# Optimization experiments

Hardware: AMD Instinct MI355X
Metric: run time of the kernel (lower is better)

Reference implementation:

```python
import jax, jax.numpy as jnp
import numpy as np

B, T, D, H = 2, 2048, 512, 8
HD = D // H
EPS = 1e-5


def setup_inputs() -> dict:
    key = jax.random.key(0)
    ks = jax.random.split(key, 8)
    s = 1.0 / np.sqrt(D)
    return {
        "x": jax.random.normal(ks[0], (B, T, D), dtype=jnp.float32),
        "Wq": jax.random.uniform(ks[1], (D, D), jnp.float32, -s, s),
        "bq": jnp.zeros((D,), jnp.float32),
        "Wk": jax.random.uniform(ks[2], (D, D), jnp.float32, -s, s),
        "bk": jnp.zeros((D,), jnp.float32),
        "Wv": jax.random.uniform(ks[3], (D, D), jnp.float32, -s, s),
        "bv": jnp.zeros((D,), jnp.float32),
        "gn_w": jnp.ones((D,), jnp.float32),
        "gn_b": jnp.zeros((D,), jnp.float32),
        "gamma": jnp.float32(0.9),
    }


def reference(x, Wq, bq, Wk, bk, Wv, bv, gn_w, gn_b, gamma):
    Bx, Tx, Dx = x.shape
    # projections (torch Linear: x @ W.T + b), split heads -> [B,H,T,hd]
    def proj(W, b):
        return (x @ W.T + b).reshape(Bx, Tx, H, HD).transpose(0, 2, 1, 3)
    Q, K, V = proj(Wq, bq), proj(Wk, bk), proj(Wv, bv)
    # retention scores with causal exponential decay mask
    attn = jnp.einsum("bhqd,bhkd->bhqk", Q, K)  # [B,H,T,T]
    idx = jnp.arange(Tx)
    diff = idx[:, None] - idx[None, :]
    # clamp negative exponents before pow to avoid inf (masked out anyway)
    decay = jnp.where(diff >= 0,
                      jnp.power(gamma, jnp.maximum(diff, 0).astype(jnp.float32)),
                      0.0)
    attn = attn * decay[None, None]
    out = jnp.einsum("bhqk,bhkd->bhqd", attn, V)  # [B,H,T,hd]
    out = out.transpose(0, 2, 1, 3)  # [B,T,H,hd]
    # GroupNorm over channels grouped by head; normalized over (T, hd) per (b, h)
    mean = out.mean(axis=(1, 3), keepdims=True)
    var = out.var(axis=(1, 3), keepdims=True)
    out = (out - mean) / jnp.sqrt(var + EPS)
    out = out.reshape(Bx, Tx, Dx) * gn_w + gn_b
    return out
```

## Files before the change

kernel.cpp:

```cpp
#include <hip/hip_runtime.h>
#include <math.h>

#define B_ 2
#define T_ 2048
#define D_ 512
#define H_ 8
#define HD_ 64
#define NG_ (B_*H_)
#define EPS_ 1e-5f

typedef __attribute__((ext_vector_type(8)))  short  short8;
typedef __attribute__((ext_vector_type(16))) float  floatx16;

__device__ inline floatx16 zero16() {
    floatx16 z;
#pragma unroll
    for (int i = 0; i < 16; i++) z[i] = 0.f;
    return z;
}

__device__ inline unsigned pack2bf(float a, float b) {
    unsigned ua = __float_as_uint(a), ub = __float_as_uint(b);
    ua = (ua + 0x7fffu + ((ua >> 16) & 1u)) >> 16;
    ub = (ub + 0x7fffu + ((ub >> 16) & 1u)) >> 16;
    return ua | (ub << 16);
}
__device__ inline short bf1(float a) {
    unsigned ua = __float_as_uint(a);
    return (short)((ua + 0x7fffu + ((ua >> 16) & 1u)) >> 16);
}
__device__ inline uint4 pack8bf(const float4& a, const float4& b) {
    uint4 o;
    o.x = pack2bf(a.x, a.y); o.y = pack2bf(a.z, a.w);
    o.z = pack2bf(b.x, b.y); o.w = pack2bf(b.z, b.w);
    return o;
}

__global__ __launch_bounds__(256, 3) void proj_mfma(
    const float* __restrict__ x,
    const float* __restrict__ Wq, const float* __restrict__ Wk, const float* __restrict__ Wv,
    const float* __restrict__ bq, const float* __restrict__ bk, const float* __restrict__ bv,
    short* __restrict__ Qo, short* __restrict__ Ko, short* __restrict__ Vto,
    float* __restrict__ stats)
{
    __shared__ short Xs[2][64 * 64];
    __shared__ short Ws2[2][128 * 64];

    const int tid = threadIdx.x;
    if (blockIdx.x == 0 && blockIdx.y == 0 && blockIdx.z == 0 && tid < 32)
        stats[tid] = 0.f;

    const int w = tid >> 6, lane = tid & 63;
    const int hi = lane >> 5, ln = lane & 31;
    const int mt0 = blockIdx.x * 64;
    const int nt0 = blockIdx.y * 128;
    const int z = blockIdx.z;
    const bool isV = (z == 2);
    const float* bias = (z == 0) ? bq : (z == 1) ? bk : bv;
    const float* Wz = (z == 0) ? Wq : (z == 1) ? Wk : Wv;

    const int srow = tid >> 3;
    const int scol = (((tid & 7) ^ ((tid >> 3) & 7)) * 8);
    const int mh = w & 1, nh = w >> 1;

    floatx16 acc[2] = {zero16(), zero16()};
    float4 xr[2][2];
    float4 wr[4][2];

    auto gload = [&](int k0) {
#pragma unroll
        for (int i = 0; i < 2; i++) {
            const float* p = x + (size_t)(mt0 + srow + i * 32) * 512 + k0 + scol;
            xr[i][0] = *(const float4*)p;
            xr[i][1] = *(const float4*)(p + 4);
        }
#pragma unroll
        for (int i = 0; i < 4; i++) {
            const float* p = Wz + (size_t)(nt0 + srow + i * 32) * 512 + k0 + scol;
            wr[i][0] = *(const float4*)p;
            wr[i][1] = *(const float4*)(p + 4);
        }
    };
    auto spill = [&](int b) {
        const int slot = (tid & 7) * 8;
#pragma unroll
        for (int i = 0; i < 2; i++)
            *(uint4*)&Xs[b][(srow + i * 32) * 64 + slot] = pack8bf(xr[i][0], xr[i][1]);
#pragma unroll
        for (int i = 0; i < 4; i++)
            *(uint4*)&Ws2[b][(srow + i * 32) * 64 + slot] = pack8bf(wr[i][0], wr[i][1]);
    };

    gload(0);
    int buf = 0;
    for (int k0 = 0; k0 < 512; k0 += 64, buf ^= 1) {
        spill(buf);
        __syncthreads();
        if (k0 + 64 < 512) gload(k0 + 64);
#pragma unroll
        for (int kk = 0; kk < 4; kk++) {
            const int gx = ((2 * kk + hi) ^ (ln & 7)) * 8;
            short8 xf = *(const short8*)(&Xs[buf][(mh * 32 + ln) * 64 + gx]);
            short8 wf[2];
#pragma unroll
            for (int s = 0; s < 2; s++)
                wf[s] = *(const short8*)(&Ws2[buf][(nh * 64 + s * 32 + ln) * 64 + gx]);
#pragma unroll
            for (int b = 0; b < 2; b++)
                acc[b] = isV
                    ? __builtin_amdgcn_mfma_f32_32x32x16_bf16(wf[b], xf, acc[b], 0, 0, 0)
                    : __builtin_amdgcn_mfma_f32_32x32x16_bf16(xf, wf[b], acc[b], 0, 0, 0);
        }
        __syncthreads();
    }

    const int head = blockIdx.y * 2 + nh;

    if (!isV) {
        short* dst = (z == 0) ? Qo : Ko;
        float bias_v[2];
#pragma unroll
        for (int b = 0; b < 2; b++) bias_v[b] = bias[nt0 + nh * 64 + b * 32 + ln];
#pragma unroll
        for (int r = 0; r < 16; r++) {
            int m = mt0 + mh * 32 + (r & 3) + 8 * (r >> 2) + 4 * hi;
            int batch = m >> 11, t = m & (T_ - 1);
            size_t rowb = ((size_t)(batch * H_ + head) * T_ + t) * HD_;
#pragma unroll
            for (int b = 0; b < 2; b++)
                dst[rowb + b * 32 + ln] = bf1(acc[b][r] + bias_v[b]);
        }
    } else {
        const int m = mt0 + mh * 32 + ln;
        const int batch = m >> 11, t = m & (T_ - 1);
#pragma unroll
        for (int b = 0; b < 2; b++) {
#pragma unroll
            for (int r = 0; r < 16; r++) {
                int chan = nt0 + nh * 64 + b * 32 + (r & 3) + 8 * (r >> 2) + 4 * hi;
                int d = chan & (HD_ - 1);
                Vto[((size_t)(batch * H_ + head) * HD_ + d) * T_ + t] = bf1(acc[b][r] + bias[chan]);
            }
        }
    }
}

__global__ __launch_bounds__(256, 2) void retention_kernel(
    const short* __restrict__ Q, const short* __restrict__ K, const short* __restrict__ Vt,
    const float* __restrict__ gamma_p,
    float* __restrict__ out,
    float* __restrict__ stats)
{
    __shared__ float red[3][32 * 64];

    const int tid  = threadIdx.x;
    const int ks   = tid >> 6, lane = tid & 63;
    const int hi   = lane >> 5, ln = lane & 31;
    const int g    = blockIdx.x, qtt = blockIdx.y;
    const int q0   = qtt * 32;
    const int qt   = qtt >> 1;

    const float gamma = gamma_p[0];
    const float lg = logf(gamma);
    int kt0 = 0;
    if (lg < -1e-6f) {
        int maxd = (int)(-13.0f / lg) + 64;
        kt0 = qt - (maxd >> 6);
        if (kt0 < 0) kt0 = 0;
    }

    const short* Qbase = Q + ((size_t)g * T_ + q0 + ln) * HD_;
    short8 qf[4];
#pragma unroll
    for (int c = 0; c < 4; c++) qf[c] = *(const short8*)(Qbase + 16 * c + 8 * hi);

    const float Alane = __expf(lg * (float)(ln - 4 * hi));
    const float G32   = __expf(-lg * 32.0f);
    float Ea[4], Eb[4];
#pragma unroll
    for (int j = 0; j < 4; j++) { Ea[j] = __expf(-lg * (float)j); Eb[j] = __expf(-lg * (float)(8 * j)); }
    const int qrel = (qtt & 1) * 32 + ln;

    floatx16 oacc[2] = {zero16(), zero16()};

    int kt = kt0 + ((ks - kt0) & 3);
    short8 kf[2][4];
    if (kt <= qt) {
        const short* Kbase = K + ((size_t)g * T_ + kt * 64) * HD_;
#pragma unroll
        for (int kh = 0; kh < 2; kh++)
#pragma unroll
            for (int c = 0; c < 4; c++)
                kf[kh][c] = *(const short8*)(Kbase + (size_t)(kh * 32 + ln) * HD_ + 16 * c + 8 * hi);
    }

    for (; kt <= qt; kt += 4) {
        const int k0 = kt * 64;

        floatx16 st[2];
#pragma unroll
        for (int kh = 0; kh < 2; kh++) {
            floatx16 acc = zero16();
#pragma unroll
            for (int c = 0; c < 4; c++)
                acc = __builtin_amdgcn_mfma_f32_32x32x16_bf16(kf[kh][c], qf[c], acc, 0, 0, 0);
            st[kh] = acc;
        }

        short8 vf[4][2];
#pragma unroll
        for (int c = 0; c < 4; c++)
#pragma unroll
            for (int dh = 0; dh < 2; dh++)
                vf[c][dh] = *(const short8*)(Vt + ((size_t)g * HD_ + dh * 32 + ln) * T_ + k0 + 16 * c + 8 * hi);

        const int ktn = kt + 4;
        if (ktn <= qt) {
            const short* Kn = K + ((size_t)g * T_ + ktn * 64) * HD_;
#pragma unroll
            for (int kh = 0; kh < 2; kh++)
#pragma unroll
                for (int c = 0; c < 4; c++)
                    kf[kh][c] = *(const short8*)(Kn + (size_t)(kh * 32 + ln) * HD_ + 16 * c + 8 * hi);
        }

        const float Ckt = __expf(lg * (float)(q0 - k0));
        const float base0 = Alane * Ckt;
        const bool diag = (kt == qt);
#pragma unroll
        for (int kh = 0; kh < 2; kh++) {
            float bb = base0 * (kh ? G32 : 1.0f);
#pragma unroll
            for (int r = 0; r < 16; r++) {
                float v = st[kh][r] * (bb * Ea[r & 3] * Eb[r >> 2]);
                if (diag) {
                    int kloc = kh * 32 + (r & 3) + 8 * (r >> 2) + 4 * hi;
                    if (qrel < kloc) v = 0.f;
                }
                st[kh][r] = v;
            }
        }

#pragma unroll
        for (int c = 0; c < 4; c++) {
            const int kh = c >> 1, rb = 8 * (c & 1);
            unsigned p0 = pack2bf(st[kh][rb+0], st[kh][rb+1]);
            unsigned p1 = pack2bf(st[kh][rb+2], st[kh][rb+3]);
            unsigned p2 = pack2bf(st[kh][rb+4], st[kh][rb+5]);
            unsigned p3 = pack2bf(st[kh][rb+6], st[kh][rb+7]);
            unsigned t0s = (unsigned)__shfl_xor((int)(hi ? p0 : p2), 32, 64);
            unsigned t1s = (unsigned)__shfl_xor((int)(hi ? p1 : p3), 32, 64);
            uint4 aw;
            aw.x = hi ? t0s : p0;  aw.y = hi ? t1s : p1;
            aw.z = hi ? p2  : t0s; aw.w = hi ? p3  : t1s;
            short8 afr = *reinterpret_cast<short8*>(&aw);
#pragma unroll
            for (int dh = 0; dh < 2; dh++)
                oacc[dh] = __builtin_amdgcn_mfma_f32_32x32x16_bf16(afr, vf[c][dh], oacc[dh], 0, 0, 0);
        }
    }

    if (ks) {
        float* rp = &red[ks - 1][0];
#pragma unroll
        for (int dh = 0; dh < 2; dh++)
#pragma unroll
            for (int r = 0; r < 16; r++) {
                int qloc = (r & 3) + 8 * (r >> 2) + 4 * hi;
                rp[qloc * 64 + dh * 32 + ln] = oacc[dh][r];
            }
    }
    __syncthreads();
    if (ks == 0) {
        const int b = g >> 3, h = g & 7;
        float sm = 0.f, sq = 0.f;
#pragma unroll
        for (int dh = 0; dh < 2; dh++)
#pragma unroll
            for (int r = 0; r < 16; r++) {
                int qloc = (r & 3) + 8 * (r >> 2) + 4 * hi;
                int col = qloc * 64 + dh * 32 + ln;
                float v = oacc[dh][r] + red[0][col] + red[1][col] + red[2][col];
                int q = q0 + qloc;
                out[((size_t)(b * T_ + q)) * D_ + h * 64 + dh * 32 + ln] = v;
                sm += v; sq += v * v;
            }
        for (int off = 32; off > 0; off >>= 1) {
            sm += __shfl_down(sm, off);
            sq += __shfl_down(sq, off);
        }
        if (lane == 0) {
            atomicAdd(&stats[g], sm);
            atomicAdd(&stats[NG_ + g], sq);
        }
    }
}

__global__ __launch_bounds__(256) void norm_kernel(
    float* __restrict__ out, const float* __restrict__ stats,
    const float* __restrict__ gn_w, const float* __restrict__ gn_b)
{
    int idx4 = blockIdx.x * 256 + threadIdx.x;
    if (idx4 >= (B_ * T_ * D_) / 4) return;
    int base = idx4 * 4;
    int c0 = base & (D_ - 1);
    int b = base >> 20;
    int g = b * H_ + (c0 >> 6);
    const float invN = 1.f / (float)(T_ * HD_);
    float mean = stats[g] * invN;
    float var  = stats[NG_ + g] * invN - mean * mean;
    float inv  = rsqrtf(var + EPS_);
    float4 v = *(float4*)&out[base];
    float4 wv = *(const float4*)&gn_w[c0];
    float4 bv = *(const float4*)&gn_b[c0];
    v.x = (v.x - mean) * inv * wv.x + bv.x;
    v.y = (v.y - mean) * inv * wv.y + bv.y;
    v.z = (v.z - mean) * inv * wv.z + bv.z;
    v.w = (v.w - mean) * inv * wv.w + bv.w;
    *(float4*)&out[base] = v;
}

extern "C" void kernel_launch(void* const* d_in, const int* in_sizes, int n_in,
                              void* d_out, int out_size, void* d_ws, size_t ws_size,
                              hipStream_t stream)
{
    const float* x    = (const float*)d_in[0];
    const float* Wq   = (const float*)d_in[1];
    const float* bq   = (const float*)d_in[2];
    const float* Wk   = (const float*)d_in[3];
    const float* bk   = (const float*)d_in[4];
    const float* Wv   = (const float*)d_in[5];
    const float* bv   = (const float*)d_in[6];
    const float* gn_w = (const float*)d_in[7];
    const float* gn_b = (const float*)d_in[8];
    const float* gam  = (const float*)d_in[9];
    float* out = (float*)d_out;

    const size_t per = (size_t)B_ * H_ * T_ * HD_;
    float* stats = (float*)d_ws;
    short* Qw  = (short*)((char*)d_ws + 256);
    short* Kw  = Qw + per;
    short* Vtw = Kw + per;

    proj_mfma<<<dim3(64, 4, 3), 256, 0, stream>>>(x, Wq, Wk, Wv, bq, bk, bv,
                                                  Qw, Kw, Vtw, stats);
    retention_kernel<<<dim3(16, 64), 256, 0, stream>>>(Qw, Kw, Vtw, gam, out, stats);
    norm_kernel<<<2048, 256, 0, stream>>>(out, stats, gn_w, gn_b);
}
```

Measured before the change: 119.9 us.

## Assign one query tile per warp in retention and drop split-K reduction

The retention kernel now gives each warp its own 32-row query tile and walks every key tile in the decay window serially. Previously the four warps of a block split the key tiles between them and combined partial results through shared memory and a barrier; that reduction is gone, and the grid shrinks to a quarter of the blocks. A redundant trailing barrier in the double-buffered projection GEMM loop is also removed. The cost is fewer resident warps per CU and longer serial per-warp loops, which may expose more memory latency.

```diff
diff --git a/kernel.cpp b/kernel.cpp
--- a/kernel.cpp
+++ b/kernel.cpp
@@ -111,7 +111,6 @@
                     ? __builtin_amdgcn_mfma_f32_32x32x16_bf16(wf[b], xf, acc[b], 0, 0, 0)
                     : __builtin_amdgcn_mfma_f32_32x32x16_bf16(xf, wf[b], acc[b], 0, 0, 0);
         }
-        __syncthreads();
     }
 
     const int head = blockIdx.y * 2 + nh;
@@ -151,12 +150,11 @@
     float* __restrict__ out,
     float* __restrict__ stats)
 {
-    __shared__ float red[3][32 * 64];
-
     const int tid  = threadIdx.x;
     const int ks   = tid >> 6, lane = tid & 63;
     const int hi   = lane >> 5, ln = lane & 31;
-    const int g    = blockIdx.x, qtt = blockIdx.y;
+    const int g    = blockIdx.x;
+    const int qtt  = blockIdx.y * 4 + ks;
     const int q0   = qtt * 32;
     const int qt   = qtt >> 1;
 
@@ -183,9 +181,9 @@
 
     floatx16 oacc[2] = {zero16(), zero16()};
 
-    int kt = kt0 + ((ks - kt0) & 3);
+    int kt = kt0;
     short8 kf[2][4];
-    if (kt <= qt) {
+    {
         const short* Kbase = K + ((size_t)g * T_ + kt * 64) * HD_;
 #pragma unroll
         for (int kh = 0; kh < 2; kh++)
@@ -194,7 +192,7 @@
                 kf[kh][c] = *(const short8*)(Kbase + (size_t)(kh * 32 + ln) * HD_ + 16 * c + 8 * hi);
     }
 
-    for (; kt <= qt; kt += 4) {
+    for (; kt <= qt; kt++) {
         const int k0 = kt * 64;
 
         floatx16 st[2];
@@ -214,9 +212,8 @@
             for (int dh = 0; dh < 2; dh++)
                 vf[c][dh] = *(const short8*)(Vt + ((size_t)g * HD_ + dh * 32 + ln) * T_ + k0 + 16 * c + 8 * hi);
 
-        const int ktn = kt + 4;
-        if (ktn <= qt) {
-            const short* Kn = K + ((size_t)g * T_ + ktn * 64) * HD_;
+        if (kt + 1 <= qt) {
+            const short* Kn = K + ((size_t)g * T_ + (kt + 1) * 64) * HD_;
 #pragma unroll
             for (int kh = 0; kh < 2; kh++)
 #pragma unroll
@@ -260,39 +257,25 @@
         }
     }
 
-    if (ks) {
-        float* rp = &red[ks - 1][0];
-#pragma unroll
-        for (int dh = 0; dh < 2; dh++)
-#pragma unroll
-            for (int r = 0; r < 16; r++) {
-                int qloc = (r & 3) + 8 * (r >> 2) + 4 * hi;
-                rp[qloc * 64 + dh * 32 + ln] = oacc[dh][r];
-            }
-    }
-    __syncthreads();
-    if (ks == 0) {
-        const int b = g >> 3, h = g & 7;
-        float sm = 0.f, sq = 0.f;
-#pragma unroll
-        for (int dh = 0; dh < 2; dh++)
-#pragma unroll
-            for (int r = 0; r < 16; r++) {
-                int qloc = (r & 3) + 8 * (r >> 2) + 4 * hi;
-                int col = qloc * 64 + dh * 32 + ln;
-                float v = oacc[dh][r] + red[0][col] + red[1][col] + red[2][col];
-                int q = q0 + qloc;
-                out[((size_t)(b * T_ + q)) * D_ + h * 64 + dh * 32 + ln] = v;
-                sm += v; sq += v * v;
-            }
-        for (int off = 32; off > 0; off >>= 1) {
-            sm += __shfl_down(sm, off);
-            sq += __shfl_down(sq, off);
-        }
-        if (lane == 0) {
-            atomicAdd(&stats[g], sm);
-            atomicAdd(&stats[NG_ + g], sq);
-        }
+    const int b = g >> 3, h = g & 7;
+    float sm = 0.f, sq = 0.f;
+#pragma unroll
+    for (int dh = 0; dh < 2; dh++)
+#pragma unroll
+        for (int r = 0; r < 16; r++) {
+            int qloc = (r & 3) + 8 * (r >> 2) + 4 * hi;
+            float v = oacc[dh][r];
+            int q = q0 + qloc;
+            out[((size_t)(b * T_ + q)) * D_ + h * 64 + dh * 32 + ln] = v;
+            sm += v; sq += v * v;
+        }
+    for (int off = 32; off > 0; off >>= 1) {
+        sm += __shfl_down(sm, off);
+        sq += __shfl_down(sq, off);
+    }
+    if (lane == 0) {
+        atomicAdd(&stats[g], sm);
+        atomicAdd(&stats[NG_ + g], sq);
     }
 }
 
@@ -344,6 +327,6 @@
 
     proj_mfma<<<dim3(64, 4, 3), 256, 0, stream>>>(x, Wq, Wk, Wv, bq, bk, bv,
                                                   Qw, Kw, Vtw, stats);
-    retention_kernel<<<dim3(16, 64), 256, 0, stream>>>(Qw, Kw, Vtw, gam, out, stats);
+    retention_kernel<<<dim3(16, 16), 256, 0, stream>>>(Qw, Kw, Vtw, gam, out, stats);
     norm_kernel<<<2048, 256, 0, stream>>>(out, stats, gn_w, gn_b);
 }
```

Result: no change. 120.5 us (+0.6%).
